# Optimization experiments

Hardware: AMD Instinct MI355X
Metric: run time of the kernel (lower is better)

Reference implementation:

```python
import jax, jax.numpy as jnp
import numpy as np

B, H, W, DIM, WS, NH, HID = 16, 64, 64, 256, 8, 8, 1024
SHIFT = WS // 2
N = WS * WS  # tokens per window


def _rel_pos_index(ws):
    coords = np.stack(np.meshgrid(np.arange(ws), np.arange(ws), indexing='ij')).reshape(2, -1)
    rel = (coords[:, :, None] - coords[:, None, :]).transpose(1, 2, 0)  # [n,n,2]
    rel[..., 0] += ws - 1
    rel[..., 1] += ws - 1
    rel[..., 0] *= 2 * ws - 1
    return rel.sum(-1)  # [n,n] ints in [0, (2ws-1)^2)


def _attn_mask(h, w, ws, ss):
    img = np.zeros((h, w), np.float32)
    cnt = 0
    sl = (slice(0, -ws), slice(-ws, -ss), slice(-ss, None))
    for hs in sl:
        for wsl in sl:
            img[hs, wsl] = cnt
            cnt += 1
    mw = img.reshape(h // ws, ws, w // ws, ws).transpose(0, 2, 1, 3).reshape(-1, ws * ws)
    d = mw[:, None, :] - mw[:, :, None]  # unsqueeze(1) - unsqueeze(2)
    return np.where(d != 0, np.float32(-100.0), np.float32(0.0))  # [nW,n,n]


RPI = jnp.asarray(_rel_pos_index(WS).reshape(-1))          # [n*n] int
MASK = jnp.asarray(_attn_mask(H, W, WS, SHIFT))            # [nW,n,n]


def ln(x, g, b, eps):
    m = x.mean(-1, keepdims=True)
    v = x.var(-1, keepdims=True)
    return (x - m) / jnp.sqrt(v + eps) * g + b


def win_part(x, ws):
    b, h, w, c = x.shape
    x = x.reshape(b, h // ws, ws, w // ws, ws, c).transpose(0, 1, 3, 2, 4, 5)
    return x.reshape(-1, ws * ws, c)  # [b*nW, n, c]


def win_rev(win, ws, h, w):
    c = win.shape[-1]
    b = win.shape[0] // ((h // ws) * (w // ws))
    x = win.reshape(b, h // ws, w // ws, ws, ws, c).transpose(0, 1, 3, 2, 4, 5)
    return x.reshape(b, h, w, c)


def attention(xw, qkv_w, qkv_b, rpb, out_w, out_b, mask):
    Bw, n, c = xw.shape
    dh = c // NH
    scale = dh ** -0.5
    qkv = (xw @ qkv_w + qkv_b).reshape(Bw, n, 3, NH, dh).transpose(2, 0, 3, 1, 4)
    q, k, v = qkv[0], qkv[1], qkv[2]                       # [Bw,NH,n,dh]
    dots = jnp.einsum('bhid,bhjd->bhij', q, k) * scale
    bias = rpb[RPI].reshape(n, n, NH).transpose(2, 0, 1)   # [NH,n,n]
    attn = dots + bias[None]
    if mask is not None:
        nW = mask.shape[0]
        attn = attn.reshape(Bw // nW, nW, NH, n, n) + mask[None, :, None]
        attn = attn.reshape(Bw, NH, n, n)
    attn = jax.nn.softmax(attn, axis=-1)
    out = jnp.einsum('bhij,bhjd->bhid', attn, v)
    out = out.transpose(0, 2, 1, 3).reshape(Bw, n, c)
    return out @ out_w + out_b


def block(x, shifted, mask, n1g, n1b, qkv_w, qkv_b, rpb, out_w, out_b,
          n2g, n2b, lng, lnb, w1, b1, w2, b2):
    b, l, c = x.shape
    shortcut = x
    x = ln(x, n1g, n1b, 1e-5).reshape(b, H, W, c)
    if shifted:
        x = jnp.roll(x, (-SHIFT, -SHIFT), (1, 2))
    xw = win_part(x, WS)
    xw = attention(xw, qkv_w, qkv_b, rpb, out_w, out_b, mask)
    x = win_rev(xw, WS, H, W)
    if shifted:
        x = jnp.roll(x, (SHIFT, SHIFT), (1, 2))
    x = shortcut + x.reshape(b, l, c)
    # FeedForward contains its own LayerNorm(eps=1e-6) after norm2 (faithful to source)
    h = ln(x, n2g, n2b, 1e-5)
    h = ln(h, lng, lnb, 1e-6)
    h = jax.nn.gelu(h @ w1 + b1, approximate=False) @ w2 + b2
    return x + h


def forward(x, *p):
    x = block(x, False, None, *p[0:15])
    x = block(x, True, MASK, *p[15:30])
    return x


def setup_inputs() -> dict:
    key = jax.random.key(0)
    ks = iter(jax.random.split(key, 16))
    s = 0.02
    d = {'x': jax.random.normal(next(ks), (B, H * W, DIM), jnp.float32)}
    for i in (0, 1):
        p = f'b{i}_'
        d[p + 'n1g'] = jnp.ones((DIM,), jnp.float32)
        d[p + 'n1b'] = jnp.zeros((DIM,), jnp.float32)
        d[p + 'qkv_w'] = jax.random.normal(next(ks), (DIM, 3 * DIM), jnp.float32) * s
        d[p + 'qkv_b'] = jnp.zeros((3 * DIM,), jnp.float32)
        d[p + 'rpb'] = jax.random.normal(next(ks), ((2 * WS - 1) ** 2, NH), jnp.float32) * s
        d[p + 'out_w'] = jax.random.normal(next(ks), (DIM, DIM), jnp.float32) * s
        d[p + 'out_b'] = jnp.zeros((DIM,), jnp.float32)
        d[p + 'n2g'] = jnp.ones((DIM,), jnp.float32)
        d[p + 'n2b'] = jnp.zeros((DIM,), jnp.float32)
        d[p + 'lng'] = jnp.ones((DIM,), jnp.float32)
        d[p + 'lnb'] = jnp.zeros((DIM,), jnp.float32)
        d[p + 'w1'] = jax.random.normal(next(ks), (DIM, HID), jnp.float32) * s
        d[p + 'b1'] = jnp.zeros((HID,), jnp.float32)
        d[p + 'w2'] = jax.random.normal(next(ks), (HID, DIM), jnp.float32) * s
        d[p + 'b2'] = jnp.zeros((DIM,), jnp.float32)
    return d


def reference(x,
              b0_n1g, b0_n1b, b0_qkv_w, b0_qkv_b, b0_rpb, b0_out_w, b0_out_b,
              b0_n2g, b0_n2b, b0_lng, b0_lnb, b0_w1, b0_b1, b0_w2, b0_b2,
              b1_n1g, b1_n1b, b1_qkv_w, b1_qkv_b, b1_rpb, b1_out_w, b1_out_b,
              b1_n2g, b1_n2b, b1_lng, b1_lnb, b1_w1, b1_b1, b1_w2, b1_b2):
    return forward(x,
                   b0_n1g, b0_n1b, b0_qkv_w, b0_qkv_b, b0_rpb, b0_out_w, b0_out_b,
                   b0_n2g, b0_n2b, b0_lng, b0_lnb, b0_w1, b0_b1, b0_w2, b0_b2,
                   b1_n1g, b1_n1b, b1_qkv_w, b1_qkv_b, b1_rpb, b1_out_w, b1_out_b,
                   b1_n2g, b1_n2b, b1_lng, b1_lnb, b1_w1, b1_b1, b1_w2, b1_b2)
```

## Files before the change

### kernel.cpp

```cpp
#include <hip/hip_runtime.h>
#include <hip/hip_bf16.h>

typedef unsigned short u16;
typedef __attribute__((ext_vector_type(8))) short bf16x8;
typedef __attribute__((ext_vector_type(8))) unsigned short u16x8;
typedef __attribute__((ext_vector_type(4))) unsigned short u16x4;
typedef __attribute__((ext_vector_type(4))) float f32x4;

__device__ inline float b2f(u16 u) {
    union { unsigned u32; float f; } x; x.u32 = ((unsigned)u) << 16; return x.f;
}
__device__ inline u16 f2b(float f) {
    return __builtin_bit_cast(u16, __float2bfloat16(f));
}

__device__ inline float fast_gelu(float v) {
    float u = v * (1.5957691216f + 0.0713548163f * v * v);
    return v * __builtin_amdgcn_rcpf(1.0f + __expf(-u));
}

#define GLOAD_LDS16(g, l) \
    __builtin_amdgcn_global_load_lds((const __attribute__((address_space(1))) void*)(const void*)(g), \
                                     (__attribute__((address_space(3))) void*)(void*)(l), 16, 0, 0)
#define FENCE() asm volatile("" ::: "memory")

__global__ __launch_bounds__(256)
void ln_win_kernel(const float* __restrict__ x, const float* __restrict__ g,
                   const float* __restrict__ b, u16* __restrict__ xw, int shift)
{
    int wid = blockIdx.x * 4 + (threadIdx.x >> 6);
    int lane = threadIdx.x & 63;
    int win = wid >> 6, tok = wid & 63;
    int bb = win >> 6, wib = win & 63;
    int h = (((wib >> 3) << 3) + (tok >> 3) + shift) & 63;
    int w = (((wib & 7) << 3) + (tok & 7) + shift) & 63;
    size_t src = ((size_t)bb * 4096 + h * 64 + w) * 256;
    float4 v = ((const float4*)(x + src))[lane];
    float s = v.x + v.y + v.z + v.w;
    float s2 = v.x*v.x + v.y*v.y + v.z*v.z + v.w*v.w;
    for (int k = 32; k > 0; k >>= 1) { s += __shfl_xor(s, k); s2 += __shfl_xor(s2, k); }
    float mean = s * (1.f/256.f);
    float var  = s2 * (1.f/256.f) - mean*mean;
    float rs = rsqrtf(var + 1e-5f);
    int c = lane * 4;
    u16x4 o;
    o[0] = f2b((v.x - mean) * rs * g[c+0] + b[c+0]);
    o[1] = f2b((v.y - mean) * rs * g[c+1] + b[c+1]);
    o[2] = f2b((v.z - mean) * rs * g[c+2] + b[c+2]);
    o[3] = f2b((v.w - mean) * rs * g[c+3] + b[c+3]);
    *(u16x4*)(xw + (size_t)wid * 256 + c) = o;
}

__global__ __launch_bounds__(256)
void ln2_kernel(const float* __restrict__ xin,
                const float* __restrict__ g1, const float* __restrict__ b1,
                const float* __restrict__ g2, const float* __restrict__ b2,
                u16* __restrict__ out)
{
    int wid = blockIdx.x * 4 + (threadIdx.x >> 6);
    int lane = threadIdx.x & 63;
    float4 v = ((const float4*)(xin + (size_t)wid * 256))[lane];
    float s = v.x + v.y + v.z + v.w;
    float s2 = v.x*v.x + v.y*v.y + v.z*v.z + v.w*v.w;
    for (int k = 32; k > 0; k >>= 1) { s += __shfl_xor(s, k); s2 += __shfl_xor(s2, k); }
    float mean = s * (1.f/256.f);
    float var  = s2 * (1.f/256.f) - mean*mean;
    float rs = rsqrtf(var + 1e-5f);
    int c = lane * 4;
    float y0 = (v.x - mean) * rs * g1[c+0] + b1[c+0];
    float y1 = (v.y - mean) * rs * g1[c+1] + b1[c+1];
    float y2 = (v.z - mean) * rs * g1[c+2] + b1[c+2];
    float y3 = (v.w - mean) * rs * g1[c+3] + b1[c+3];
    float t = y0 + y1 + y2 + y3;
    float t2 = y0*y0 + y1*y1 + y2*y2 + y3*y3;
    for (int k = 32; k > 0; k >>= 1) { t += __shfl_xor(t, k); t2 += __shfl_xor(t2, k); }
    float m2 = t * (1.f/256.f);
    float v2 = t2 * (1.f/256.f) - m2*m2;
    float rs2 = rsqrtf(v2 + 1e-6f);
    u16x4 o;
    o[0] = f2b((y0 - m2) * rs2 * g2[c+0] + b2[c+0]);
    o[1] = f2b((y1 - m2) * rs2 * g2[c+1] + b2[c+1]);
    o[2] = f2b((y2 - m2) * rs2 * g2[c+2] + b2[c+2]);
    o[3] = f2b((y3 - m2) * rs2 * g2[c+3] + b2[c+3]);
    *(u16x4*)(out + (size_t)wid * 256 + c) = o;
}

__global__ __launch_bounds__(256)
void transpose_w(const float* __restrict__ W, u16* __restrict__ Wt, int K, int N)
{
    __shared__ float t[32][33];
    int nb = blockIdx.x * 32, kb = blockIdx.y * 32;
    int tx = threadIdx.x & 31, ty = threadIdx.x >> 5;
    #pragma unroll
    for (int r = 0; r < 32; r += 8)
        t[ty + r][tx] = W[(size_t)(kb + ty + r) * N + nb + tx];
    __syncthreads();
    #pragma unroll
    for (int r = 0; r < 32; r += 8)
        Wt[(size_t)(nb + ty + r) * K + kb + tx] = f2b(t[tx][ty + r]);
}

__global__ __launch_bounds__(256)
void build_bias(const float* __restrict__ rpb, float* __restrict__ bmT)
{
    int idx = blockIdx.x * 256 + threadIdx.x;
    int q = idx & 63, k = (idx >> 6) & 63, h = (idx >> 12) & 7, cls = idx >> 15;
    int qh = q >> 3, qw = q & 7, kh = k >> 3, kw = k & 7;
    float v = rpb[((qh - kh + 7) * 15 + (qw - kw + 7)) * 8 + h];
    int ch = cls >> 1, cw = cls & 1;
    int rq = (ch ? (qh < 4 ? 1 : 2) : 0) * 3 + (cw ? (qw < 4 ? 1 : 2) : 0);
    int rk = (ch ? (kh < 4 ? 1 : 2) : 0) * 3 + (cw ? (kw < 4 ? 1 : 2) : 0);
    if (rq != rk) v -= 100.f;
    bmT[idx] = v * 1.4426950408889634f;
}

template<int EPI>
__global__ __launch_bounds__(256, 2)
void areg_gemm(const u16* __restrict__ A, const u16* __restrict__ Bt,
               const float* __restrict__ bias, void* __restrict__ out,
               const float* __restrict__ resid, int N, int shift)
{
    constexpr int K = 256;
    __shared__ u16 Bs[2][8][64][32];
    const int tid = threadIdx.x, lane = tid & 63, wv = tid >> 6;
    const int g = lane >> 4, r = lane & 15;
    const int bid = blockIdx.x;
    const int bm = (bid & 7) * 64 + (bid >> 3);
    const int row0 = bm * 128 + wv * 32;

    bf16x8 af[2][8];
    #pragma unroll
    for (int rf = 0; rf < 2; ++rf)
        #pragma unroll
        for (int ks = 0; ks < 8; ++ks)
            af[rf][ks] = *(const bf16x8*)(A + (size_t)(row0 + rf * 16 + r) * K + ks * 32 + g * 8);

    const int NB = N >> 6;
#define STAGE(bn_, buf_) do { \
        _Pragma("unroll") \
        for (int it = 0; it < 8; ++it) { \
            const int S = it * 256 + wv * 64 + lane; \
            const int ks_ = S >> 8, col_ = (S >> 2) & 63; \
            const int k8_ = (S & 3) ^ (col_ & 3) ^ ((col_ >> 2) & 1); \
            GLOAD_LDS16(Bt + (size_t)((bn_) * 64 + col_) * K + ks_ * 32 + k8_ * 8, \
                        &Bs[buf_][0][0][0] + (size_t)(it * 256 + wv * 64) * 8); \
        } \
    } while (0)

    const int rc = (g ^ (r & 3) ^ ((r >> 2) & 1)) * 8;

    FENCE();
    STAGE(0, 0);
    for (int bn = 0; bn < NB; ++bn) {
        const int cur = bn & 1;
        if (bn + 1 < NB) { STAGE(bn + 1, cur ^ 1); }
        if (bn == 0) {
            asm volatile("s_waitcnt vmcnt(8)" ::: "memory");
        } else if (bn + 1 < NB) {
            if (EPI == 2) asm volatile("s_waitcnt vmcnt(24)" ::: "memory");
            else          asm volatile("s_waitcnt vmcnt(16)" ::: "memory");
        } else {
            if (EPI == 2) asm volatile("s_waitcnt vmcnt(16)" ::: "memory");
            else          asm volatile("s_waitcnt vmcnt(8)" ::: "memory");
        }
        __builtin_amdgcn_s_barrier();
        FENCE();
        f32x4 acc[4][2] = {};
        #pragma unroll
        for (int ks = 0; ks < 8; ++ks) {
            bf16x8 bf[4];
            #pragma unroll
            for (int cf = 0; cf < 4; ++cf)
                bf[cf] = *(const bf16x8*)(&Bs[cur][ks][cf * 16 + r][rc]);
            __builtin_amdgcn_s_setprio(1);
            #pragma unroll
            for (int cf = 0; cf < 4; ++cf)
                #pragma unroll
                for (int rf = 0; rf < 2; ++rf)
                    acc[cf][rf] = __builtin_amdgcn_mfma_f32_16x16x32_bf16(bf[cf], af[rf][ks], acc[cf][rf], 0, 0, 0);
            __builtin_amdgcn_s_setprio(0);
        }
        asm volatile("s_waitcnt lgkmcnt(0)" ::: "memory");
        __builtin_amdgcn_sched_barrier(0);
        __builtin_amdgcn_s_barrier();
        FENCE();
        #pragma unroll
        for (int rf = 0; rf < 2; ++rf) {
            const int row = row0 + rf * 16 + r;
            size_t orow;
            if (EPI == 2) {
                int win = row >> 6, tok = row & 63;
                int bb = win >> 6, wib = win & 63;
                int h = (((wib >> 3) << 3) + (tok >> 3) + shift) & 63;
                int w = (((wib & 7) << 3) + (tok & 7) + shift) & 63;
                orow = (size_t)bb * 4096 + h * 64 + w;
            } else {
                orow = (size_t)row;
            }
            #pragma unroll
            for (int cf = 0; cf < 4; ++cf) {
                const int colb = bn * 64 + cf * 16 + g * 4;
                const f32x4 bv = *(const f32x4*)(bias + colb);
                if (EPI == 0) {
                    u16x4 o;
                    #pragma unroll
                    for (int e = 0; e < 4; ++e) o[e] = f2b(acc[cf][rf][e] + bv[e]);
                    *(u16x4*)((u16*)out + (size_t)row * N + colb) = o;
                } else if (EPI == 1) {
                    u16x4 o;
                    #pragma unroll
                    for (int e = 0; e < 4; ++e) o[e] = f2b(fast_gelu(acc[cf][rf][e] + bv[e]));
                    *(u16x4*)((u16*)out + (size_t)row * N + colb) = o;
                } else {
                    const f32x4 rv = *(const f32x4*)(resid + orow * N + colb);
                    f32x4 o;
                    #pragma unroll
                    for (int e = 0; e < 4; ++e) o[e] = rv[e] + acc[cf][rf][e] + bv[e];
                    *(f32x4*)((float*)out + orow * N + colb) = o;
                }
            }
        }
        FENCE();
    }
#undef STAGE
}

__global__ __launch_bounds__(256)
void gemm_k4(const u16* __restrict__ A, const u16* __restrict__ Bt,
             const float* __restrict__ bias, float* __restrict__ out,
             const float* __restrict__ resid, int M, int N, int K)
{
    __shared__ u16 As[4][128][32];
    __shared__ u16 Bs[4][128][32];
    const int tid = threadIdx.x, lane = tid & 63, wv = tid >> 6;
    const int g = lane >> 4, r = lane & 15;
    const int wr = wv >> 1, wc = wv & 1;
    const int nwg = gridDim.x * gridDim.y;
    const int lid = blockIdx.y * gridDim.x + blockIdx.x;
    const int qq = nwg >> 3, r8 = nwg & 7;
    const int xcd = lid & 7, pos = lid >> 3;
    const int nid = (xcd < r8 ? xcd * (qq + 1) : r8 * (qq + 1) + (xcd - r8) * qq) + pos;
    const int bm = nid / gridDim.x, bn = nid % gridDim.x;
    f32x4 acc[4][4] = {};
    const int arow = wv * 16 + (lane >> 2);
    const int scol = (((lane & 3) ^ ((lane >> 2) & 3) ^ ((lane >> 4) & 1)) * 8);
    const u16* gA = A + (size_t)(bm * 128 + arow) * K + scol;
    const u16* gB = Bt + (size_t)(bn * 128 + arow) * K + scol;
    const int nk = K >> 5;
    const int rc = (g ^ (r & 3) ^ ((r >> 2) & 1)) * 8;

#define STAGE(t) do { \
        u16* a_ = &As[(t) & 3][0][0]; u16* b_ = &Bs[(t) & 3][0][0]; \
        GLOAD_LDS16(gA + (size_t)(t) * 32,                    a_ + wv * 512); \
        GLOAD_LDS16(gA + (size_t)(t) * 32 + (size_t)64 * K,   a_ + 2048 + wv * 512); \
        GLOAD_LDS16(gB + (size_t)(t) * 32,                    b_ + wv * 512); \
        GLOAD_LDS16(gB + (size_t)(t) * 32 + (size_t)64 * K,   b_ + 2048 + wv * 512); \
    } while (0)

    STAGE(0);
    STAGE(1);
    for (int kt = 0; kt < nk; ++kt) {
        const int cur = kt & 3;
        if (kt + 2 < nk) {
            STAGE(kt + 2);
            asm volatile("s_waitcnt vmcnt(8)" ::: "memory");
        } else if (kt + 1 < nk) {
            asm volatile("s_waitcnt vmcnt(4)" ::: "memory");
        } else {
            asm volatile("s_waitcnt vmcnt(0)" ::: "memory");
        }
        __builtin_amdgcn_s_barrier();
        FENCE();
        bf16x8 af[4], bf[4];
        #pragma unroll
        for (int i = 0; i < 4; ++i)
            af[i] = *(const bf16x8*)(&As[cur][wr * 64 + i * 16 + r][rc]);
        #pragma unroll
        for (int j = 0; j < 4; ++j)
            bf[j] = *(const bf16x8*)(&Bs[cur][wc * 64 + j * 16 + r][rc]);
        __builtin_amdgcn_s_setprio(1);
        #pragma unroll
        for (int j = 0; j < 4; ++j)
            #pragma unroll
            for (int i = 0; i < 4; ++i)
                acc[j][i] = __builtin_amdgcn_mfma_f32_16x16x32_bf16(bf[j], af[i], acc[j][i], 0, 0, 0);
        __builtin_amdgcn_s_setprio(0);
        asm volatile("s_waitcnt lgkmcnt(0)" ::: "memory");
        __builtin_amdgcn_sched_barrier(0);
    }
#undef STAGE

    #pragma unroll
    for (int i = 0; i < 4; ++i) {
        const int row = bm * 128 + wr * 64 + i * 16 + r;
        #pragma unroll
        for (int j = 0; j < 4; ++j) {
            const int colb = bn * 128 + wc * 64 + j * 16 + g * 4;
            const f32x4 bv = *(const f32x4*)(bias + colb);
            const f32x4 rv = *(const f32x4*)(resid + (size_t)row * N + colb);
            f32x4 o;
            #pragma unroll
            for (int e = 0; e < 4; ++e) o[e] = rv[e] + acc[j][i][e] + bv[e];
            *(f32x4*)(out + (size_t)row * N + colb) = o;
        }
    }
}

template<int SHIFTED>
__global__ __launch_bounds__(256)
void attn_mfma(const u16* __restrict__ qkv, const float* __restrict__ bmT,
               u16* __restrict__ out)
{
    __shared__ u16 pbuf[4][64 * 72];
    __shared__ u16 vbuf[4][32 * 72];
    const int tid = threadIdx.x, lane = tid & 63, wv = tid >> 6;
    const int g = lane >> 4, r = lane & 15;
    const int win = blockIdx.x;
    u16* P  = pbuf[wv];
    u16* Vt = vbuf[wv];
    const u16* base = qkv + (size_t)win * 64 * 768;
    int cls = 0;
    if (SHIFTED) {
        int wib = win & 63;
        cls = (((wib >> 3) == 7) ? 2 : 0) + (((wib & 7) == 7) ? 1 : 0);
    }
    const float sc = 0.17677669529663687f * 1.4426950408889634f;

    for (int hh = 0; hh < 2; ++hh) {
        const int h = wv * 2 + hh;
        const float* bmh = bmT + ((size_t)cls * 8 + h) * 4096;
        bf16x8 kf[4], qf[4];
        #pragma unroll
        for (int i = 0; i < 4; ++i) {
            kf[i] = *(const bf16x8*)(base + (size_t)(i * 16 + r) * 768 + 256 + h * 32 + g * 8);
            qf[i] = *(const bf16x8*)(base + (size_t)(i * 16 + r) * 768 +       h * 32 + g * 8);
        }
        #pragma unroll
        for (int d0 = 0; d0 < 32; d0 += 8) {
            u16x8 vv = *(const u16x8*)(base + (size_t)lane * 768 + 512 + h * 32 + d0);
            #pragma unroll
            for (int e = 0; e < 8; ++e) Vt[(d0 + e) * 72 + lane] = vv[e];
        }
        f32x4 acc[4][4] = {};
        #pragma unroll
        for (int i = 0; i < 4; ++i)
            #pragma unroll
            for (int j = 0; j < 4; ++j)
                acc[i][j] = __builtin_amdgcn_mfma_f32_16x16x32_bf16(kf[i], qf[j], acc[i][j], 0, 0, 0);
        #pragma unroll
        for (int i = 0; i < 4; ++i) {
            const int kb = (i * 16 + g * 4) * 64;
            #pragma unroll
            for (int j = 0; j < 4; ++j) {
                const int qq = j * 16 + r;
                #pragma unroll
                for (int rr = 0; rr < 4; ++rr)
                    acc[i][j][rr] = acc[i][j][rr] * sc + bmh[kb + rr * 64 + qq];
            }
        }
        float inv_[4];
        #pragma unroll
        for (int j = 0; j < 4; ++j) {
            float m = acc[0][j][0];
            #pragma unroll
            for (int i = 0; i < 4; ++i)
                #pragma unroll
                for (int rr = 0; rr < 4; ++rr) m = fmaxf(m, acc[i][j][rr]);
            m = fmaxf(m, __shfl_xor(m, 16));
            m = fmaxf(m, __shfl_xor(m, 32));
            float s = 0.f;
            #pragma unroll
            for (int i = 0; i < 4; ++i)
                #pragma unroll
                for (int rr = 0; rr < 4; ++rr) {
                    float p = exp2f(acc[i][j][rr] - m);
                    acc[i][j][rr] = p; s += p;
                }
            s += __shfl_xor(s, 16);
            s += __shfl_xor(s, 32);
            inv_[j] = 1.f / s;
        }
        #pragma unroll
        for (int j = 0; j < 4; ++j) {
            const float iv = inv_[j];
            #pragma unroll
            for (int i = 0; i < 4; ++i) {
                u16x4 w;
                #pragma unroll
                for (int rr = 0; rr < 4; ++rr) w[rr] = f2b(acc[i][j][rr] * iv);
                *(u16x4*)(P + (j * 16 + r) * 72 + i * 16 + g * 4) = w;
            }
        }
        f32x4 o[2][4] = {};
        #pragma unroll
        for (int ks = 0; ks < 2; ++ks) {
            bf16x8 pa[4], vb[2];
            #pragma unroll
            for (int i = 0; i < 4; ++i)
                pa[i] = *(const bf16x8*)(P + (i * 16 + r) * 72 + ks * 32 + g * 8);
            #pragma unroll
            for (int j = 0; j < 2; ++j)
                vb[j] = *(const bf16x8*)(Vt + (j * 16 + r) * 72 + ks * 32 + g * 8);
            #pragma unroll
            for (int j = 0; j < 2; ++j)
                #pragma unroll
                for (int i = 0; i < 4; ++i)
                    o[j][i] = __builtin_amdgcn_mfma_f32_16x16x32_bf16(vb[j], pa[i], o[j][i], 0, 0, 0);
        }
        u16* op = out + (size_t)win * 64 * 256 + h * 32;
        #pragma unroll
        for (int i = 0; i < 4; ++i) {
            const int qrow = i * 16 + r;
            #pragma unroll
            for (int j = 0; j < 2; ++j) {
                u16x4 w;
                #pragma unroll
                for (int rr = 0; rr < 4; ++rr) w[rr] = f2b(o[j][i][rr]);
                *(u16x4*)(op + (size_t)qrow * 256 + j * 16 + g * 4) = w;
            }
        }
    }
}

extern "C" void kernel_launch(void* const* d_in, const int* in_sizes, int n_in,
                              void* d_out, int out_size, void* d_ws, size_t ws_size,
                              hipStream_t stream)
{
    (void)in_sizes; (void)n_in; (void)out_size; (void)ws_size;
    const float* x = (const float*)d_in[0];
    char* ws = (char*)d_ws;
    size_t off = 0;
    auto alloc = [&](size_t bytes) { void* p = ws + off; off += (bytes + 255) & ~(size_t)255; return p; };

    u16 *wtq[2], *wto[2], *wt1[2], *wt2[2];
    float* bmT[2];
    for (int i = 0; i < 2; ++i) {
        wtq[i] = (u16*)alloc((size_t)768 * 256 * 2);
        wto[i] = (u16*)alloc((size_t)256 * 256 * 2);
        wt1[i] = (u16*)alloc((size_t)1024 * 256 * 2);
        wt2[i] = (u16*)alloc((size_t)256 * 1024 * 2);
        bmT[i] = (float*)alloc((size_t)4 * 8 * 64 * 64 * 4);
    }
    u16*  xw  = (u16*)alloc((size_t)65536 * 256 * 2);
    u16*  big = (u16*)alloc((size_t)65536 * 1024 * 2);
    float* x1 = (float*)alloc((size_t)65536 * 256 * 4);
    float* outp = (float*)d_out;

    for (int blk = 0; blk < 2; ++blk) {
        const float* const* P = (const float* const*)(d_in + 1 + blk * 15);
        transpose_w<<<dim3(768 / 32, 256 / 32), 256, 0, stream>>>(P[2], wtq[blk], 256, 768);
        transpose_w<<<dim3(256 / 32, 256 / 32), 256, 0, stream>>>(P[5], wto[blk], 256, 256);
        transpose_w<<<dim3(1024 / 32, 256 / 32), 256, 0, stream>>>(P[11], wt1[blk], 256, 1024);
        transpose_w<<<dim3(256 / 32, 1024 / 32), 256, 0, stream>>>(P[13], wt2[blk], 1024, 256);
        build_bias<<<512, 256, 0, stream>>>(P[4], bmT[blk]);
    }

    for (int blk = 0; blk < 2; ++blk) {
        const float* const* P = (const float* const*)(d_in + 1 + blk * 15);
        const int sh = blk ? 4 : 0;
        const float* xin = blk ? outp : x;

        ln_win_kernel<<<16384, 256, 0, stream>>>(xin, P[0], P[1], xw, sh);
        areg_gemm<0><<<512, 256, 0, stream>>>(xw, wtq[blk], P[3], big, nullptr, 768, 0);
        if (blk) attn_mfma<1><<<1024, 256, 0, stream>>>(big, bmT[blk], xw);
        else     attn_mfma<0><<<1024, 256, 0, stream>>>(big, bmT[blk], xw);
        areg_gemm<2><<<512, 256, 0, stream>>>(xw, wto[blk], P[6], x1, xin, 256, sh);
        ln2_kernel<<<16384, 256, 0, stream>>>(x1, P[7], P[8], P[9], P[10], xw);
        areg_gemm<1><<<512, 256, 0, stream>>>(xw, wt1[blk], P[12], big, nullptr, 1024, 0);
        gemm_k4<<<dim3(2, 512), 256, 0, stream>>>(big, wt2[blk], P[14], outp, x1, 65536, 256, 1024);
    }
}
```

Baseline: 686.3 us.

## Replace fc2 GEMM with full-width 128x256 tile, 512-thread blocks, BK=64 double buffer

The second MLP GEMM (K=1024, N=256) now uses one 512-thread workgroup per 128-row strip covering the whole output width. Each A strip is read from global memory once instead of twice. The K-loop moves to 64-wide steps with double buffering instead of 32-wide steps with a 4-deep ring, and adds a second barrier per iteration. Block index mapping is swizzled across XCDs. In exchange, pipeline depth drops and LDS use per block grows (96KB), which may limit occupancy.

```diff
diff --git a/kernel.cpp b/kernel.cpp
--- a/kernel.cpp
+++ b/kernel.cpp
@@ -225,83 +225,92 @@
 #undef STAGE
 }
 
-__global__ __launch_bounds__(256)
-void gemm_k4(const u16* __restrict__ A, const u16* __restrict__ Bt,
-             const float* __restrict__ bias, float* __restrict__ out,
-             const float* __restrict__ resid, int M, int N, int K)
-{
-    __shared__ u16 As[4][128][32];
-    __shared__ u16 Bs[4][128][32];
+__global__ __launch_bounds__(512)
+void gemm_full(const u16* __restrict__ A, const u16* __restrict__ Bt,
+               const float* __restrict__ bias, float* __restrict__ out,
+               const float* __restrict__ resid, int K)
+{
+    constexpr int N = 256;
+    __shared__ u16 As[2][2][128][32];
+    __shared__ u16 Bs[2][2][256][32];
     const int tid = threadIdx.x, lane = tid & 63, wv = tid >> 6;
     const int g = lane >> 4, r = lane & 15;
-    const int wr = wv >> 1, wc = wv & 1;
-    const int nwg = gridDim.x * gridDim.y;
-    const int lid = blockIdx.y * gridDim.x + blockIdx.x;
-    const int qq = nwg >> 3, r8 = nwg & 7;
-    const int xcd = lid & 7, pos = lid >> 3;
-    const int nid = (xcd < r8 ? xcd * (qq + 1) : r8 * (qq + 1) + (xcd - r8) * qq) + pos;
-    const int bm = nid / gridDim.x, bn = nid % gridDim.x;
+    const int wr = wv >> 2, wc = wv & 3;
+    const int bid = blockIdx.x;
+    const int bm = (bid & 7) * 64 + (bid >> 3);
+    const u16* gA = A + (size_t)bm * 128 * K;
+
+#define STAGE(kt_, buf_) do { \
+        _Pragma("unroll") \
+        for (int it = 0; it < 2; ++it) { \
+            const int L = it * 512 + tid; \
+            const int kk_ = L >> 9, row_ = (L >> 2) & 127, s_ = L & 3; \
+            const int c8 = s_ ^ (row_ & 3) ^ ((row_ >> 2) & 1); \
+            GLOAD_LDS16(gA + (size_t)row_ * K + (kt_) * 64 + kk_ * 32 + c8 * 8, \
+                        &As[buf_][0][0][0] + (size_t)L * 8); \
+        } \
+        _Pragma("unroll") \
+        for (int it = 0; it < 4; ++it) { \
+            const int L = it * 512 + tid; \
+            const int kk_ = L >> 10, row_ = (L >> 2) & 255, s_ = L & 3; \
+            const int c8 = s_ ^ (row_ & 3) ^ ((row_ >> 2) & 1); \
+            GLOAD_LDS16(Bt + (size_t)row_ * K + (kt_) * 64 + kk_ * 32 + c8 * 8, \
+                        &Bs[buf_][0][0][0] + (size_t)L * 8); \
+        } \
+    } while (0)
+
+    const int rc = (g ^ (r & 3) ^ ((r >> 2) & 1)) * 8;
     f32x4 acc[4][4] = {};
-    const int arow = wv * 16 + (lane >> 2);
-    const int scol = (((lane & 3) ^ ((lane >> 2) & 3) ^ ((lane >> 4) & 1)) * 8);
-    const u16* gA = A + (size_t)(bm * 128 + arow) * K + scol;
-    const u16* gB = Bt + (size_t)(bn * 128 + arow) * K + scol;
-    const int nk = K >> 5;
-    const int rc = (g ^ (r & 3) ^ ((r >> 2) & 1)) * 8;
-
-#define STAGE(t) do { \
-        u16* a_ = &As[(t) & 3][0][0]; u16* b_ = &Bs[(t) & 3][0][0]; \
-        GLOAD_LDS16(gA + (size_t)(t) * 32,                    a_ + wv * 512); \
-        GLOAD_LDS16(gA + (size_t)(t) * 32 + (size_t)64 * K,   a_ + 2048 + wv * 512); \
-        GLOAD_LDS16(gB + (size_t)(t) * 32,                    b_ + wv * 512); \
-        GLOAD_LDS16(gB + (size_t)(t) * 32 + (size_t)64 * K,   b_ + 2048 + wv * 512); \
-    } while (0)
-
-    STAGE(0);
-    STAGE(1);
+    const int nk = K >> 6;
+
+    FENCE();
+    STAGE(0, 0);
     for (int kt = 0; kt < nk; ++kt) {
-        const int cur = kt & 3;
-        if (kt + 2 < nk) {
-            STAGE(kt + 2);
-            asm volatile("s_waitcnt vmcnt(8)" ::: "memory");
-        } else if (kt + 1 < nk) {
-            asm volatile("s_waitcnt vmcnt(4)" ::: "memory");
+        const int cur = kt & 1;
+        if (kt + 1 < nk) {
+            STAGE(kt + 1, cur ^ 1);
+            asm volatile("s_waitcnt vmcnt(6)" ::: "memory");
         } else {
             asm volatile("s_waitcnt vmcnt(0)" ::: "memory");
         }
         __builtin_amdgcn_s_barrier();
         FENCE();
-        bf16x8 af[4], bf[4];
-        #pragma unroll
-        for (int i = 0; i < 4; ++i)
-            af[i] = *(const bf16x8*)(&As[cur][wr * 64 + i * 16 + r][rc]);
-        #pragma unroll
-        for (int j = 0; j < 4; ++j)
-            bf[j] = *(const bf16x8*)(&Bs[cur][wc * 64 + j * 16 + r][rc]);
-        __builtin_amdgcn_s_setprio(1);
-        #pragma unroll
-        for (int j = 0; j < 4; ++j)
+        #pragma unroll
+        for (int kk = 0; kk < 2; ++kk) {
+            bf16x8 af[4], bf[4];
             #pragma unroll
             for (int i = 0; i < 4; ++i)
-                acc[j][i] = __builtin_amdgcn_mfma_f32_16x16x32_bf16(bf[j], af[i], acc[j][i], 0, 0, 0);
-        __builtin_amdgcn_s_setprio(0);
+                af[i] = *(const bf16x8*)(&As[cur][kk][wr * 64 + i * 16 + r][rc]);
+            #pragma unroll
+            for (int j = 0; j < 4; ++j)
+                bf[j] = *(const bf16x8*)(&Bs[cur][kk][wc * 64 + j * 16 + r][rc]);
+            __builtin_amdgcn_s_setprio(1);
+            #pragma unroll
+            for (int j = 0; j < 4; ++j)
+                #pragma unroll
+                for (int i = 0; i < 4; ++i)
+                    acc[j][i] = __builtin_amdgcn_mfma_f32_16x16x32_bf16(bf[j], af[i], acc[j][i], 0, 0, 0);
+            __builtin_amdgcn_s_setprio(0);
+        }
         asm volatile("s_waitcnt lgkmcnt(0)" ::: "memory");
         __builtin_amdgcn_sched_barrier(0);
+        __builtin_amdgcn_s_barrier();
+        FENCE();
     }
 #undef STAGE
 
     #pragma unroll
     for (int i = 0; i < 4; ++i) {
-        const int row = bm * 128 + wr * 64 + i * 16 + r;
+        const size_t row = (size_t)bm * 128 + wr * 64 + i * 16 + r;
         #pragma unroll
         for (int j = 0; j < 4; ++j) {
-            const int colb = bn * 128 + wc * 64 + j * 16 + g * 4;
+            const int colb = wc * 64 + j * 16 + g * 4;
             const f32x4 bv = *(const f32x4*)(bias + colb);
-            const f32x4 rv = *(const f32x4*)(resid + (size_t)row * N + colb);
+            const f32x4 rv = *(const f32x4*)(resid + row * N + colb);
             f32x4 o;
             #pragma unroll
             for (int e = 0; e < 4; ++e) o[e] = rv[e] + acc[j][i][e] + bv[e];
-            *(f32x4*)(out + (size_t)row * N + colb) = o;
+            *(f32x4*)(out + row * N + colb) = o;
         }
     }
 }
@@ -467,6 +476,6 @@
         areg_gemm<2><<<512, 256, 0, stream>>>(xw, wto[blk], P[6], x1, xin, 256, sh);
         ln2_kernel<<<16384, 256, 0, stream>>>(x1, P[7], P[8], P[9], P[10], xw);
         areg_gemm<1><<<512, 256, 0, stream>>>(xw, wt1[blk], P[12], big, nullptr, 1024, 0);
-        gemm_k4<<<dim3(2, 512), 256, 0, stream>>>(big, wt2[blk], P[14], outp, x1, 65536, 256, 1024);
-    }
-}
+        gemm_full<<<512, 512, 0, stream>>>(big, wt2[blk], P[14], outp, x1, 1024);
+    }
+}
```

Result: slower. 705.9 us (+2.9%).
